# Optimization experiments

Measured on AMD Instinct MI355X. Metric: run time of the kernel, lower is better.

Reference implementation:

```python
import jax, jax.numpy as jnp
import numpy as np
import math

B, L, C, D, H, NLAYERS, DFF = 256, 100, 55, 512, 8, 3, 64


def _pos_embedding(length, d_model):
    pos = np.arange(length, dtype=np.float32)[:, None]
    div = np.exp(np.arange(0, d_model, 2, dtype=np.float32) * (-math.log(10000.0) / d_model))
    pe = np.zeros((length, d_model), dtype=np.float32)
    pe[:, 0::2] = np.sin(pos * div)
    pe[:, 1::2] = np.cos(pos * div)
    return jnp.asarray(pe)


def setup_inputs() -> dict:
    key = jax.random.key(0)
    ks = jax.random.split(key, 12)
    r = lambda k, s, sc: jax.random.normal(k, s, dtype=jnp.float32) * sc
    sD = 1.0 / math.sqrt(D)
    return {
        'x': r(ks[0], (B, L, C), 1.0),
        'tok_w': r(ks[1], (D, C, 3), 1.0 / math.sqrt(3 * C)),  # Conv1d(c_in->d_model, k=3, circular, no bias)
        'pe': _pos_embedding(L, D),
        'Wq': r(ks[2], (NLAYERS, D, D), sD), 'bq': jnp.zeros((NLAYERS, D), jnp.float32),
        'Wk': r(ks[3], (NLAYERS, D, D), sD), 'bk': jnp.zeros((NLAYERS, D), jnp.float32),
        'Wv': r(ks[4], (NLAYERS, D, D), sD), 'bv': jnp.zeros((NLAYERS, D), jnp.float32),
        'Wsig': r(ks[5], (NLAYERS, H, D), sD), 'bsig': jnp.zeros((NLAYERS, H), jnp.float32),
        'Wo': r(ks[6], (NLAYERS, D, D), sD), 'bo': jnp.zeros((NLAYERS, D), jnp.float32),
        'W1': r(ks[7], (NLAYERS, DFF, D), sD), 'b1': jnp.zeros((NLAYERS, DFF), jnp.float32),  # conv1 (1x1)
        'W2': r(ks[8], (NLAYERS, D, DFF), 1.0 / math.sqrt(DFF)), 'b2': jnp.zeros((NLAYERS, D), jnp.float32),  # conv2 (1x1)
        'proj_w': r(ks[9], (C, D), sD), 'proj_b': jnp.zeros((C,), jnp.float32),
    }


def _forward(x, tok_w, pe, Wq, bq, Wk, bk, Wv, bv, Wsig, bsig, Wo, bo, W1, b1, W2, b2, proj_w, proj_b):
    Bx, Lx, _ = x.shape
    nlayers, nH = Wsig.shape[0], Wsig.shape[1]
    d_model = Wq.shape[1]
    dk = d_model // nH
    scale = 1.0 / math.sqrt(dk)
    # token embedding: circular-padded Conv1d(k=3, no bias), then + positional embedding
    xc = jnp.pad(jnp.swapaxes(x, 1, 2), ((0, 0), (0, 0), (1, 1)), mode='wrap')  # [B,C,L+2]
    emb = jax.lax.conv_general_dilated(xc, tok_w, (1,), 'VALID', dimension_numbers=('NCW', 'OIW', 'NCW'))
    h = jnp.swapaxes(emb, 1, 2) + pe[None]  # [B,L,D]
    dist = jnp.abs(jnp.arange(Lx)[:, None] - jnp.arange(Lx)[None, :]).astype(h.dtype)  # |i-j|
    for l in range(nlayers):
        q = h @ Wq[l].T + bq[l]                       # [B,L,D]
        k = (h @ Wk[l].T + bk[l]).reshape(Bx, Lx, nH, dk)
        v = (h @ Wv[l].T + bv[l]).reshape(Bx, Lx, nH, dk)
        # NOTE: source applies sigma projection to the *projected* queries
        sigma = q @ Wsig[l].T + bsig[l]               # [B,L,H]
        qh = q.reshape(Bx, Lx, nH, dk)
        scores = jnp.einsum('blhe,bshe->bhls', qh, k)  # [B,H,L,L]
        series = jax.nn.softmax(scale * scores, axis=-1)
        # Gaussian prior branch (mask_flag=False; computed in source forward,
        # does not feed the module's returned output)
        sg = jnp.swapaxes(sigma, 1, 2)                 # [B,H,L]
        sg = jnp.power(3.0, jax.nn.sigmoid(sg * 5.0) + 1e-5) - 1.0
        sgE = sg[..., None]                            # [B,H,L,1]
        _prior = jnp.exp(-(dist ** 2)[None, None] / (2.0 * sgE ** 2)) / (math.sqrt(2.0 * math.pi) * sgE)
        o = jnp.einsum('bhls,bshd->blhd', series, v).reshape(Bx, Lx, d_model)
        h = h + (o @ Wo[l].T + bo[l])                  # residual 1 (dropout=identity at eval)
        y = jax.nn.gelu(h @ W1[l].T + b1[l], approximate=False)  # conv1 1x1 + gelu
        h = h + (y @ W2[l].T + b2[l])                  # conv2 1x1, residual 2
    return h @ proj_w.T + proj_b                       # [B,L,c_out]


def reference(x, tok_w, pe, Wq, bq, Wk, bk, Wv, bv, Wsig, bsig, Wo, bo, W1, b1, W2, b2, proj_w, proj_b):
    return _forward(x, tok_w, pe, Wq, bq, Wk, bk, Wv, bv, Wsig, bsig, Wo, bo, W1, b1, W2, b2, proj_w, proj_b)
```

## Files before the change

kernel.cpp:

```cpp
#include <hip/hip_runtime.h>
#include <stdint.h>

typedef unsigned short u16;
typedef __attribute__((ext_vector_type(8))) short short8;
typedef __attribute__((ext_vector_type(4))) float f32x4;

#define DEVI __device__ __forceinline__

#define BB   256
#define LL   100
#define CC   55
#define DD   512
#define HH   8
#define DKK  64
#define MM   (BB * LL)
#define KEMB 192
#define NSEG 17

DEVI float bf2f(u16 s) { union { unsigned int u; float f; } x; x.u = ((unsigned int)s) << 16; return x.f; }
DEVI u16 f2bf(float f) {
  union { float f; unsigned int u; } x; x.f = f;
  unsigned int u = x.u;
  return (u16)((u + 0x7FFFu + ((u >> 16) & 1u)) >> 16);
}

DEVI void async_lds16(const u16* gp, u16* lp) {
  __builtin_amdgcn_global_load_lds((const __attribute__((address_space(1))) void*)gp,
                                   (__attribute__((address_space(3))) void*)lp, 16, 0, 0);
}

DEVI void wave_lds_fence() {
  asm volatile("s_waitcnt lgkmcnt(0)" ::: "memory");
  __builtin_amdgcn_wave_barrier();
}

DEVI int swz_row(int r) { return (r & 3) ^ ((r >> 2) & 3); }

__global__ void detect_dtype(const u16* __restrict__ x, int* __restrict__ flag) {
  __shared__ int cnt[256];
  int tid = threadIdx.x;
  u16 u = x[2 * tid];
  int e = (u >> 7) & 0xFF;
  cnt[tid] = (e >= 0x5F && e <= 0x90) ? 1 : 0;
  __syncthreads();
  for (int s = 128; s > 0; s >>= 1) { if (tid < s) cnt[tid] += cnt[tid + s]; __syncthreads(); }
  if (tid == 0) *flag = (cnt[0] >= 160) ? 0 : 1;
}

struct Segs { const void* src[NSEG]; int off[NSEG + 1]; };

__global__ void convert_all(Segs s, const int* __restrict__ flag, u16* __restrict__ dst) {
  int i = blockIdx.x * 256 + threadIdx.x;
  if (i >= s.off[NSEG]) return;
  int sidx = 0;
#pragma unroll
  for (int k = 1; k < NSEG; k++) if (i >= s.off[k]) sidx = k;
  int j = i - s.off[sidx];
  u16 v;
  if (*flag) v = f2bf(((const float*)s.src[sidx])[j]);
  else       v = ((const u16*)s.src[sidx])[j];
  dst[i] = v;
}

__global__ void repack_w(const u16* __restrict__ tokw, u16* __restrict__ Wg) {
  int idx = blockIdx.x * 256 + threadIdx.x;
  if (idx >= 512 * KEMB) return;
  int d = idx / KEMB, j = idx % KEMB, k = j >> 6, c = j & 63;
  Wg[idx] = (c < CC) ? tokw[d * (CC * 3) + c * 3 + k] : (u16)0;
}

__global__ void repack_x(const u16* __restrict__ x, u16* __restrict__ Xg) {
  int idx = blockIdx.x * 256 + threadIdx.x;
  if (idx >= MM * KEMB) return;
  int m = idx / KEMB, j = idx % KEMB, k = j >> 6, c = j & 63;
  int b = m / LL, l = m % LL;
  int l2 = l + k - 1; l2 = (l2 + LL) % LL;
  Xg[idx] = (c < CC) ? x[(size_t)(b * LL + l2) * CC + c] : (u16)0;
}

struct GemmW { const u16* W[3]; const u16* bias[3]; void* out[3]; };

template<int BM, int BN, int NTT, int TAG, bool QKV, bool DIRECT>
__global__ __launch_bounds__(256)
void gemm_bt(const u16* __restrict__ A, int K, GemmW w,
             const u16* __restrict__ pe,
             const u16* __restrict__ resid,
             int dogelu,
             int ldo, int nvalid,
             const int* __restrict__ dtf)
{
  constexpr int BK = 32;
  constexpr int MI = BM / 32;
  constexpr int CW = BN / 2, NT = CW / 16;
  constexpr int SW = CW + 4;
  constexpr int STAGE_U16 = (BM + BN) * BK * 2;
  __shared__ alignas(16) u16 smem[STAGE_U16];
  u16* As = smem;
  u16* Bs = smem + BM * BK * 2;

  const int tid = threadIdx.x;
  const int lane = tid & 63;
  const int wv = __builtin_amdgcn_readfirstlane(tid >> 6);
  const int wm = wv & 1, wn = wv >> 1;
  const int l15 = lane & 15, qd = lane >> 4;
  const int swz = swz_row(l15);

  const int id = blockIdx.x;
  const int mpx = gridDim.x / (NTT * 8);
  const int xcd = id & 7, slot = id >> 3;
  const int m_t = xcd * mpx + slot / NTT;
  const int n_t = slot % NTT;
  const int m0 = m_t * BM;
  int n0 = n_t * BN;
  int sel = 0, n0l = n0;
  if (QKV) { sel = n0 >> 9; n0l = n0 & 511; }
  const u16* W = w.W[sel];
  const u16* bias = w.bias[sel];
  void* outp = w.out[sel];

  const f32x4 zf = {0.f, 0.f, 0.f, 0.f};
  f32x4 acc[MI][NT];
#pragma unroll
  for (int i = 0; i < MI; i++)
#pragma unroll
    for (int j = 0; j < NT; j++) acc[i][j] = zf;

  for (int k0 = 0; k0 < K; k0 += 2 * BK) {
    __syncthreads();
#pragma unroll
    for (int p = 0; p < 2; p++) {
      u16* Asp = As + p * BM * BK;
      u16* Bsp = Bs + p * BN * BK;
      const int kp = k0 + p * BK;
#pragma unroll
      for (int i = 0; i < BM / 64; i++) {
        int base = i * 256 + wv * 64;
        int idx = base + lane;
        int row = idx >> 2;
        int cs = ((idx & 3) ^ swz_row(row)) * 8;
        async_lds16(A + (size_t)(m0 + row) * K + kp + cs, Asp + base * 8);
      }
#pragma unroll
      for (int i = 0; i < BN / 64; i++) {
        int base = i * 256 + wv * 64;
        int idx = base + lane;
        int row = idx >> 2;
        int cs = ((idx & 3) ^ swz_row(row)) * 8;
        int gr = n0l + row; if (gr >= nvalid) gr = nvalid - 1;
        async_lds16(W + (size_t)gr * K + kp + cs, Bsp + base * 8);
      }
    }
    __syncthreads();

#pragma unroll
    for (int p = 0; p < 2; p++) {
      const u16* Asp = As + p * BM * BK;
      const u16* Bsp = Bs + p * BN * BK;
      short8 af[MI], bfr[NT];
#pragma unroll
      for (int mi = 0; mi < MI; mi++)
        af[mi] = *(const short8*)&Asp[(wm * (BM / 2) + mi * 16 + l15) * BK + ((qd ^ swz) * 8)];
#pragma unroll
      for (int ni = 0; ni < NT; ni++)
        bfr[ni] = *(const short8*)&Bsp[(wn * CW + ni * 16 + l15) * BK + ((qd ^ swz) * 8)];
#pragma unroll
      for (int mi = 0; mi < MI; mi++)
#pragma unroll
        for (int ni = 0; ni < NT; ni++)
          acc[mi][ni] = __builtin_amdgcn_mfma_f32_16x16x32_bf16(af[mi], bfr[ni], acc[mi][ni], 0, 0, 0);
    }
  }

  if (DIRECT) {
    const int sf = (dtf != nullptr) ? *dtf : 0;
#pragma unroll
    for (int mi = 0; mi < MI; mi++)
#pragma unroll
      for (int ni = 0; ni < NT; ni++) {
        int gcol = n0l + wn * CW + ni * 16 + l15;
        float bv = (bias && gcol < nvalid) ? bf2f(bias[gcol]) : 0.f;
#pragma unroll
        for (int r = 0; r < 4; r++) {
          int grow = m0 + wm * (BM / 2) + mi * 16 + qd * 4 + r;
          if (gcol < nvalid) {
            float v = acc[mi][ni][r] + bv;
            if (sf) ((float*)outp)[(size_t)grow * ldo + gcol] = v;
            else    ((u16*)outp)[(size_t)grow * ldo + gcol] = f2bf(v);
          }
        }
      }
    return;
  }

  __syncthreads();
  u16* slab = smem + wv * 16 * SW;
#pragma unroll
  for (int mi = 0; mi < MI; mi++) {
    const int lr = wm * (BM / 2) + mi * 16 + qd * 4;
    float v[NT][4];
    if (!QKV && resid) {
#pragma unroll
      for (int ni = 0; ni < NT; ni++) {
        int col = n0l + wn * CW + ni * 16 + l15;
#pragma unroll
        for (int r = 0; r < 4; r++)
          v[ni][r] = bf2f(resid[(size_t)(m0 + lr + r) * DD + col]);
      }
    } else {
#pragma unroll
      for (int ni = 0; ni < NT; ni++)
#pragma unroll
        for (int r = 0; r < 4; r++) v[ni][r] = 0.f;
    }
#pragma unroll
    for (int ni = 0; ni < NT; ni++) {
      const int lc = wn * CW + ni * 16 + l15;
      float bv = bias ? bf2f(bias[n0l + lc]) : 0.f;
#pragma unroll
      for (int r = 0; r < 4; r++) {
        float x = v[ni][r] + acc[mi][ni][r] + bv;
        if (!QKV && pe) x += bf2f(pe[((m0 + lr + r) % LL) * DD + n0l + lc]);
        if (!QKV && dogelu) x = 0.5f * x * (1.f + erff(x * 0.70710678118654752f));
        v[ni][r] = x;
      }
    }
#pragma unroll
    for (int ni = 0; ni < NT; ni++)
#pragma unroll
      for (int r = 0; r < 4; r++)
        slab[(qd * 4 + r) * SW + ni * 16 + l15] = f2bf(v[ni][r]);
    wave_lds_fence();
    if (BN == 128) {
      int r2 = lane >> 2, c2 = (lane & 3) * 16;
      int grow = m0 + wm * (BM / 2) + mi * 16 + r2;
      u16* op = (u16*)outp + (size_t)grow * ldo + n0l + wn * CW + c2;
      *(short8*)&op[0] = *(const short8*)&slab[r2 * SW + c2];
      *(short8*)&op[8] = *(const short8*)&slab[r2 * SW + c2 + 8];
    } else {
      if (lane < 32) {
        int r2 = lane >> 1, c2 = (lane & 1) * 16;
        int grow = m0 + wm * (BM / 2) + mi * 16 + r2;
        u16* op = (u16*)outp + (size_t)grow * ldo + n0l + wn * CW + c2;
        *(short8*)&op[0] = *(const short8*)&slab[r2 * SW + c2];
        *(short8*)&op[8] = *(const short8*)&slab[r2 * SW + c2 + 8];
      }
    }
    wave_lds_fence();
  }
}

__global__ __launch_bounds__(512)
void gemm_qkv(const u16* __restrict__ A, GemmW w)
{
  constexpr int K = DD;
  constexpr int NBK = K >> 5;
  constexpr int SLOT = 12288;
  __shared__ alignas(16) u16 smem[3 * SLOT];

  const int tid = threadIdx.x;
  const int lane = tid & 63;
  const int wv = __builtin_amdgcn_readfirstlane(tid >> 6);
  const int wm = wv & 1, wn = wv >> 1;
  const int l15 = lane & 15, qd = lane >> 4;
  const int swk = ((qd ^ swz_row(l15)) & 3) * 8;

  const int id = blockIdx.x;
  const int mpx = gridDim.x / 48;
  const int xcd = id & 7, sl = id >> 3;
  const int m_t = xcd * mpx + sl / 6;
  const int n_t = sl % 6;
  const int m0 = m_t * 128;
  const int sel = n_t >> 1;
  const int n0l = (n_t & 1) * 256;
  const u16* W = w.W[sel];
  const u16* bias = w.bias[sel];
  u16* outp = (u16*)w.out[sel];

  const int arow = tid >> 2;
  const u16* a_src = A + (size_t)(m0 + arow) * K + ((tid & 3) ^ swz_row(arow)) * 8;
  const int br0 = tid >> 2, br1 = 128 + (tid >> 2);
  const u16* b_src0 = W + (size_t)(n0l + br0) * K + ((tid & 3) ^ swz_row(br0)) * 8;
  const u16* b_src1 = W + (size_t)(n0l + br1) * K + ((tid & 3) ^ swz_row(br1)) * 8;
  const int a_dst  = wv * 512;
  const int b_dst0 = 4096 + wv * 512;
  const int b_dst1 = 8192 + wv * 512;

  auto STAGE = [&](int t) {
    u16* sb = smem + (t % 3) * SLOT;
    const int kp = t << 5;
    async_lds16(a_src + kp,  sb + a_dst);
    async_lds16(b_src0 + kp, sb + b_dst0);
    async_lds16(b_src1 + kp, sb + b_dst1);
  };

  const f32x4 zf = {0.f, 0.f, 0.f, 0.f};
  f32x4 acc[4][4];
#pragma unroll
  for (int i = 0; i < 4; i++)
#pragma unroll
    for (int j = 0; j < 4; j++) acc[i][j] = zf;

  STAGE(0);
  STAGE(1);
  for (int s = 0; s < NBK; ++s) {
    if (s + 1 < NBK) {
      asm volatile("s_waitcnt vmcnt(3)" ::: "memory");
    } else {
      asm volatile("s_waitcnt vmcnt(0)" ::: "memory");
    }
    __builtin_amdgcn_s_barrier();
    asm volatile("" ::: "memory");
    if (s + 2 < NBK) STAGE(s + 2);
    const u16* sb = smem + (s % 3) * SLOT;
    short8 af[4], bf[4];
#pragma unroll
    for (int mi = 0; mi < 4; mi++)
      af[mi] = *(const short8*)&sb[(wm * 64 + mi * 16 + l15) * 32 + swk];
#pragma unroll
    for (int ni = 0; ni < 4; ni++)
      bf[ni] = *(const short8*)&sb[4096 + (wn * 64 + ni * 16 + l15) * 32 + swk];
#pragma unroll
    for (int mi = 0; mi < 4; mi++)
#pragma unroll
      for (int ni = 0; ni < 4; ni++)
        acc[mi][ni] = __builtin_amdgcn_mfma_f32_16x16x32_bf16(af[mi], bf[ni], acc[mi][ni], 0, 0, 0);
    asm volatile("s_waitcnt lgkmcnt(0)" ::: "memory");
  }
  __syncthreads();

  u16* slab = smem + wv * 4608;
#pragma unroll
  for (int mi = 0; mi < 4; mi++)
#pragma unroll
    for (int ni = 0; ni < 4; ni++) {
      float bv = bf2f(bias[n0l + wn * 64 + ni * 16 + l15]);
#pragma unroll
      for (int r = 0; r < 4; r++)
        slab[(mi * 16 + qd * 4 + r) * 72 + ni * 16 + l15] = f2bf(acc[mi][ni][r] + bv);
    }
  wave_lds_fence();
  {
    const int srow = lane >> 3, chk = lane & 7;
#pragma unroll
    for (int j = 0; j < 8; j++) {
      int row = j * 8 + srow;
      int grow = m0 + wm * 64 + row;
      u16* op = outp + (size_t)grow * DD + n0l + wn * 64 + chk * 8;
      *(short8*)op = *(const short8*)&slab[row * 72 + chk * 8];
    }
  }
}

__global__ __launch_bounds__(512)
void gemm_wo(const u16* __restrict__ A, const u16* __restrict__ W,
             const u16* __restrict__ bias, const u16* __restrict__ resid,
             u16* __restrict__ outp)
{
  constexpr int K = DD;
  constexpr int NBK = K >> 5;
  constexpr int SLOT = 8192;
  __shared__ alignas(16) u16 smem[3 * SLOT];

  const int tid = threadIdx.x;
  const int lane = tid & 63;
  const int wv = __builtin_amdgcn_readfirstlane(tid >> 6);
  const int wm = wv & 1, wn = wv >> 1;
  const int l15 = lane & 15, qd = lane >> 4;
  const int swk = ((qd ^ swz_row(l15)) & 3) * 8;

  const int id = blockIdx.x;
  const int mpx = gridDim.x >> 5;
  const int xcd = id & 7, sl = id >> 3;
  const int m_t = xcd * mpx + (sl >> 2);
  const int m0 = m_t * 128;
  const int n0l = (sl & 3) * 128;

  const int prow = tid >> 2;
  const int pcs = ((tid & 3) ^ swz_row(prow)) * 8;
  const u16* a_src = A + (size_t)(m0 + prow) * K + pcs;
  const u16* b_src = W + (size_t)(n0l + prow) * K + pcs;
  const int a_dst = wv * 512;
  const int b_dst = 4096 + wv * 512;

  auto STAGE = [&](int t) {
    u16* sb = smem + (t % 3) * SLOT;
    const int kp = t << 5;
    async_lds16(a_src + kp, sb + a_dst);
    async_lds16(b_src + kp, sb + b_dst);
  };

  const f32x4 zf = {0.f, 0.f, 0.f, 0.f};
  f32x4 acc[4][2];
#pragma unroll
  for (int i = 0; i < 4; i++)
#pragma unroll
    for (int j = 0; j < 2; j++) acc[i][j] = zf;

  STAGE(0);
  STAGE(1);
  for (int s = 0; s < NBK; ++s) {
    if (s + 1 < NBK) {
      asm volatile("s_waitcnt vmcnt(2)" ::: "memory");
    } else {
      asm volatile("s_waitcnt vmcnt(0)" ::: "memory");
    }
    __builtin_amdgcn_s_barrier();
    asm volatile("" ::: "memory");
    if (s + 2 < NBK) STAGE(s + 2);
    const u16* sb = smem + (s % 3) * SLOT;
    short8 af[4], bf[2];
#pragma unroll
    for (int mi = 0; mi < 4; mi++)
      af[mi] = *(const short8*)&sb[(wm * 64 + mi * 16 + l15) * 32 + swk];
#pragma unroll
    for (int ni = 0; ni < 2; ni++)
      bf[ni] = *(const short8*)&sb[4096 + (wn * 32 + ni * 16 + l15) * 32 + swk];
#pragma unroll
    for (int mi = 0; mi < 4; mi++)
#pragma unroll
      for (int ni = 0; ni < 2; ni++)
        acc[mi][ni] = __builtin_amdgcn_mfma_f32_16x16x32_bf16(af[mi], bf[ni], acc[mi][ni], 0, 0, 0);
    asm volatile("s_waitcnt lgkmcnt(0)" ::: "memory");
  }
  __syncthreads();

  u16* slab = smem + wv * 2304;
#pragma unroll
  for (int mi = 0; mi < 4; mi++)
#pragma unroll
    for (int ni = 0; ni < 2; ni++) {
      const int col = n0l + wn * 32 + ni * 16 + l15;
      float bv = bf2f(bias[col]);
#pragma unroll
      for (int r = 0; r < 4; r++) {
        const int grow = m0 + wm * 64 + mi * 16 + qd * 4 + r;
        float x = acc[mi][ni][r] + bv + bf2f(resid[(size_t)grow * DD + col]);
        slab[(mi * 16 + qd * 4 + r) * 36 + ni * 16 + l15] = f2bf(x);
      }
    }
  wave_lds_fence();
  {
    const int srow = lane >> 2, chk = lane & 3;
#pragma unroll
    for (int j = 0; j < 4; j++) {
      int row = j * 16 + srow;
      int grow = m0 + wm * 64 + row;
      u16* op = outp + (size_t)grow * DD + n0l + wn * 32 + chk * 8;
      *(short8*)op = *(const short8*)&slab[row * 36 + chk * 8];
    }
  }
}

__global__ __launch_bounds__(256)
void ffn_fused(const u16* __restrict__ h, const u16* __restrict__ W1,
               const u16* __restrict__ b1, const u16* __restrict__ W2,
               const u16* __restrict__ b2, u16* __restrict__ hout)
{
  constexpr int BM = 64, BK = 32, SW = 36;
  __shared__ alignas(16) u16 smem[4096 + 10496];
  u16* y      = smem;
  u16* shared = smem + 4096;
  u16* As  = shared;
  u16* Bs  = shared + 4096;
  u16* Bs2 = shared;
  u16* slabs = shared + 8192;

  const int tid = threadIdx.x;
  const int lane = tid & 63;
  const int wv = __builtin_amdgcn_readfirstlane(tid >> 6);
  const int wm = wv & 1, wn = wv >> 1;
  const int l15 = lane & 15, qd = lane >> 4;
  const int swz = swz_row(l15);
  const int id = blockIdx.x;
  const int mpx = gridDim.x >> 3;
  const int lid = (id & 7) * mpx + (id >> 3);
  const int m0 = (lid >> 1) * BM;
  const int nh = lid & 1;

  const int srow = tid >> 2;
  const int scs = ((tid & 3) ^ swz_row(srow)) * 8;
  const f32x4 zf = {0.f, 0.f, 0.f, 0.f};

  f32x4 acc[2][2];
#pragma unroll
  for (int i = 0; i < 2; i++)
#pragma unroll
    for (int j = 0; j < 2; j++) acc[i][j] = zf;

  for (int k0 = 0; k0 < DD; k0 += 64) {
    __syncthreads();
#pragma unroll
    for (int p = 0; p < 2; p++) {
      const int kp = k0 + p * BK;
      async_lds16(h  + (size_t)(m0 + srow) * DD + kp + scs, As + p * 2048 + tid * 8);
      async_lds16(W1 + (size_t)srow * DD + kp + scs,        Bs + p * 2048 + tid * 8);
    }
    __syncthreads();
#pragma unroll
    for (int p = 0; p < 2; p++) {
      short8 af[2], bfr[2];
#pragma unroll
      for (int mi = 0; mi < 2; mi++)
        af[mi] = *(const short8*)&As[p * 2048 + (wm * 32 + mi * 16 + l15) * BK + ((qd ^ swz) * 8)];
#pragma unroll
      for (int ni = 0; ni < 2; ni++)
        bfr[ni] = *(const short8*)&Bs[p * 2048 + (wn * 32 + ni * 16 + l15) * BK + ((qd ^ swz) * 8)];
#pragma unroll
      for (int mi = 0; mi < 2; mi++)
#pragma unroll
        for (int ni = 0; ni < 2; ni++)
          acc[mi][ni] = __builtin_amdgcn_mfma_f32_16x16x32_bf16(af[mi], bfr[ni], acc[mi][ni], 0, 0, 0);
    }
  }
#pragma unroll
  for (int mi = 0; mi < 2; mi++)
#pragma unroll
    for (int ni = 0; ni < 2; ni++) {
      float bv = bf2f(b1[wn * 32 + ni * 16 + l15]);
#pragma unroll
      for (int r = 0; r < 4; r++) {
        int row = wm * 32 + mi * 16 + qd * 4 + r;
        int kpos = ni * 16 + l15;
        int slot = ((kpos >> 3) ^ swz_row(row)) & 3;
        float x = acc[mi][ni][r] + bv;
        x = 0.5f * x * (1.f + erff(x * 0.70710678118654752f));
        y[wn * 2048 + row * BK + slot * 8 + (kpos & 7)] = f2bf(x);
      }
    }
  __syncthreads();

  auto stage2 = [&](int buf, int nc) {
#pragma unroll
    for (int p = 0; p < 2; p++)
      async_lds16(W2 + (size_t)(nc * 64 + srow) * 64 + p * BK + scs,
                  Bs2 + buf * 4096 + p * 2048 + tid * 8);
  };
  const int nc0 = nh * 4, nc1 = nc0 + 4;
  stage2(0, nc0);
  int cur = 0;
  u16* slab = slabs + wv * 16 * SW;
  for (int nc = nc0; nc < nc1; nc++) {
    __syncthreads();
    if (nc + 1 < nc1) stage2(cur ^ 1, nc + 1);
    f32x4 a2[2][2];
#pragma unroll
    for (int i = 0; i < 2; i++)
#pragma unroll
      for (int j = 0; j < 2; j++) a2[i][j] = zf;
#pragma unroll
    for (int p = 0; p < 2; p++) {
      short8 af[2], bfr[2];
#pragma unroll
      for (int mi = 0; mi < 2; mi++)
        af[mi] = *(const short8*)&y[p * 2048 + (wm * 32 + mi * 16 + l15) * BK + ((qd ^ swz) * 8)];
#pragma unroll
      for (int ni = 0; ni < 2; ni++)
        bfr[ni] = *(const short8*)&Bs2[cur * 4096 + p * 2048 + (wn * 32 + ni * 16 + l15) * BK + ((qd ^ swz) * 8)];
#pragma unroll
      for (int mi = 0; mi < 2; mi++)
#pragma unroll
        for (int ni = 0; ni < 2; ni++)
          a2[mi][ni] = __builtin_amdgcn_mfma_f32_16x16x32_bf16(af[mi], bfr[ni], a2[mi][ni], 0, 0, 0);
    }
    const int n0l = nc * 64;
#pragma unroll
    for (int mi = 0; mi < 2; mi++) {
      const int lr = wm * 32 + mi * 16 + qd * 4;
      float v[2][4];
#pragma unroll
      for (int ni = 0; ni < 2; ni++) {
        int col = n0l + wn * 32 + ni * 16 + l15;
        float bv = bf2f(b2[col]);
#pragma unroll
        for (int r = 0; r < 4; r++)
          v[ni][r] = bf2f(h[(size_t)(m0 + lr + r) * DD + col]) + a2[mi][ni][r] + bv;
      }
#pragma unroll
      for (int ni = 0; ni < 2; ni++)
#pragma unroll
        for (int r = 0; r < 4; r++)
          slab[(qd * 4 + r) * SW + ni * 16 + l15] = f2bf(v[ni][r]);
      wave_lds_fence();
      if (lane < 32) {
        int r2 = lane >> 1, c2 = (lane & 1) * 16;
        int grow = m0 + wm * 32 + mi * 16 + r2;
        u16* op = hout + (size_t)grow * DD + n0l + wn * 32 + c2;
        *(short8*)&op[0] = *(const short8*)&slab[r2 * SW + c2];
        *(short8*)&op[8] = *(const short8*)&slab[r2 * SW + c2 + 8];
      }
      wave_lds_fence();
    }
    cur ^= 1;
  }
}

__global__ __launch_bounds__(256)
void attn(const u16* __restrict__ qg, const u16* __restrict__ kg,
          const u16* __restrict__ vg, u16* __restrict__ og)
{
  constexpr int LP = 128;
  __shared__ alignas(16) u16 Ks[LP * DKK];
  __shared__ alignas(16) u16 Vt[DKK * LP];

  const int bh = blockIdx.x;
  const int b = bh >> 3, h = bh & 7;
  const size_t base = (size_t)b * LL * DD + (size_t)h * DKK;
  const int tid = threadIdx.x, lane = tid & 63, wv = tid >> 6;
  const int l15 = lane & 15, qd = lane >> 4;
  const short8 z8 = {0, 0, 0, 0, 0, 0, 0, 0};

  for (int i = tid; i < LP * 8; i += 256) {
    int row = i >> 3, e8 = (i & 7) * 8;
    short8 val = z8;
    if (row < LL) val = *(const short8*)(kg + base + (size_t)row * DD + e8);
    *(short8*)&Ks[row * DKK + e8] = val;
  }
  for (int i = tid; i < LP * 8; i += 256) {
    int j = i & 127, d0 = (i >> 7) * 8;
    short8 val = z8;
    if (j < LL) val = *(const short8*)(vg + base + (size_t)j * DD + d0);
#pragma unroll
    for (int u = 0; u < 8; u++) Vt[(d0 + u) * LP + j] = (u16)val[u];
  }
  __syncthreads();

  const f32x4 zf = {0.f, 0.f, 0.f, 0.f};
  f32x4 sc[2][8];
#pragma unroll
  for (int it = 0; it < 2; it++)
#pragma unroll
    for (int jt = 0; jt < 8; jt++) sc[it][jt] = zf;

  short8 af[2][2];
#pragma unroll
  for (int it = 0; it < 2; it++) {
    int row = (2 * wv + it) * 16 + l15;
#pragma unroll
    for (int ks = 0; ks < 2; ks++) {
      short8 val = z8;
      if (row < LL) val = *(const short8*)(qg + base + (size_t)row * DD + ks * 32 + qd * 8);
      af[it][ks] = val;
    }
  }
#pragma unroll
  for (int jt = 0; jt < 8; jt++) {
    short8 b0 = *(const short8*)&Ks[(jt * 16 + l15) * DKK + qd * 8];
    short8 b1 = *(const short8*)&Ks[(jt * 16 + l15) * DKK + 32 + qd * 8];
#pragma unroll
    for (int it = 0; it < 2; it++) {
      sc[it][jt] = __builtin_amdgcn_mfma_f32_16x16x32_bf16(af[it][0], b0, sc[it][jt], 0, 0, 0);
      sc[it][jt] = __builtin_amdgcn_mfma_f32_16x16x32_bf16(af[it][1], b1, sc[it][jt], 0, 0, 0);
    }
  }

  constexpr float scale = 0.125f;
#pragma unroll
  for (int it = 0; it < 2; it++) {
#pragma unroll
    for (int r = 0; r < 4; r++) {
      float vals[8];
      float mx = -1e30f;
#pragma unroll
      for (int jt = 0; jt < 8; jt++) {
        int col = jt * 16 + l15;
        float vv = sc[it][jt][r] * scale;
        if (col >= LL) vv = -1e30f;
        vals[jt] = vv;
        mx = fmaxf(mx, vv);
      }
#pragma unroll
      for (int off = 1; off < 16; off <<= 1) mx = fmaxf(mx, __shfl_xor(mx, off, 64));
      float s = 0.f;
#pragma unroll
      for (int jt = 0; jt < 8; jt++) { float p = __expf(vals[jt] - mx); vals[jt] = p; s += p; }
#pragma unroll
      for (int off = 1; off < 16; off <<= 1) s += __shfl_xor(s, off, 64);
      float inv = 1.f / s;
#pragma unroll
      for (int jt = 0; jt < 8; jt++) sc[it][jt][r] = vals[jt] * inv;
    }
  }
  __syncthreads();

  u16* Pc = Ks;
  f32x4 oc[2][4];
#pragma unroll
  for (int it = 0; it < 2; it++)
#pragma unroll
    for (int dt = 0; dt < 4; dt++) oc[it][dt] = zf;

#pragma unroll
  for (int it = 0; it < 2; it++) {
    int rb = (2 * wv + it) * 16 + qd * 4;
#pragma unroll
    for (int r = 0; r < 4; r++)
#pragma unroll
      for (int jt = 0; jt < 4; jt++)
        Pc[(rb + r) * DKK + jt * 16 + l15] = f2bf(sc[it][jt][r]);
  }
  __syncthreads();
#pragma unroll
  for (int ks = 0; ks < 2; ks++) {
    short8 ap[2];
#pragma unroll
    for (int it = 0; it < 2; it++)
      ap[it] = *(const short8*)&Pc[((2 * wv + it) * 16 + l15) * DKK + ks * 32 + qd * 8];
#pragma unroll
    for (int dt = 0; dt < 4; dt++) {
      short8 bv = *(const short8*)&Vt[(dt * 16 + l15) * LP + ks * 32 + qd * 8];
#pragma unroll
      for (int it = 0; it < 2; it++)
        oc[it][dt] = __builtin_amdgcn_mfma_f32_16x16x32_bf16(ap[it], bv, oc[it][dt], 0, 0, 0);
    }
  }
  __syncthreads();

#pragma unroll
  for (int it = 0; it < 2; it++) {
    int rb = (2 * wv + it) * 16 + qd * 4;
#pragma unroll
    for (int r = 0; r < 4; r++)
#pragma unroll
      for (int jt = 4; jt < 8; jt++)
        Pc[(rb + r) * DKK + (jt - 4) * 16 + l15] = f2bf(sc[it][jt][r]);
  }
  __syncthreads();
#pragma unroll
  for (int ks = 2; ks < 4; ks++) {
    short8 ap[2];
#pragma unroll
    for (int it = 0; it < 2; it++)
      ap[it] = *(const short8*)&Pc[((2 * wv + it) * 16 + l15) * DKK + (ks - 2) * 32 + qd * 8];
#pragma unroll
    for (int dt = 0; dt < 4; dt++) {
      short8 bv = *(const short8*)&Vt[(dt * 16 + l15) * LP + ks * 32 + qd * 8];
#pragma unroll
      for (int it = 0; it < 2; it++)
        oc[it][dt] = __builtin_amdgcn_mfma_f32_16x16x32_bf16(ap[it], bv, oc[it][dt], 0, 0, 0);
    }
  }

  __syncthreads();
  u16* Os = Ks;
#pragma unroll
  for (int it = 0; it < 2; it++) {
    int rb = (2 * wv + it) * 16 + qd * 4;
#pragma unroll
    for (int dt = 0; dt < 4; dt++)
#pragma unroll
      for (int r = 0; r < 4; r++)
        Os[(rb + r) * DKK + dt * 16 + l15] = f2bf(oc[it][dt][r]);
  }
  __syncthreads();
  {
    int row = tid >> 1, c0 = (tid & 1) * 32;
    if (row < LL) {
      u16* op = og + base + (size_t)row * DD + c0;
#pragma unroll
      for (int c = 0; c < 32; c += 8)
        *(short8*)&op[c] = *(const short8*)&Os[row * DKK + c0 + c];
    }
  }
}

extern "C" void kernel_launch(void* const* d_in, const int* in_sizes, int n_in,
                              void* d_out, int out_size, void* d_ws, size_t ws_size,
                              hipStream_t stream)
{
  (void)in_sizes; (void)n_in; (void)out_size; (void)ws_size;

  char* ws = (char*)d_ws;
  size_t off = 0;
  auto alloc = [&](size_t bytes) { char* p = ws + off; off += (bytes + 255) & ~(size_t)255; return p; };
  int* dflag = (int*)alloc(256);
  static const int seg_sizes[NSEG] = {
    MM * CC, DD * CC * 3, LL * DD,
    3 * DD * DD, 3 * DD, 3 * DD * DD, 3 * DD, 3 * DD * DD, 3 * DD,
    3 * DD * DD, 3 * DD, 3 * 64 * DD, 3 * 64, 3 * DD * 64, 3 * DD,
    CC * DD, CC
  };
  static const int seg_input[NSEG] = {0, 1, 2, 3, 4, 5, 6, 7, 8, 11, 12, 13, 14, 15, 16, 17, 18};
  int total = 0, segoff[NSEG + 1];
  for (int i = 0; i < NSEG; i++) { segoff[i] = total; total += seg_sizes[i]; }
  segoff[NSEG] = total;
  u16* canon = (u16*)alloc((size_t)total * 2);

  u16* hbf = (u16*)alloc((size_t)MM * DD * 2);
  u16* h2  = (u16*)alloc((size_t)MM * DD * 2);
  u16* qb  = (u16*)alloc((size_t)MM * DD * 2);
  u16* kb  = (u16*)alloc((size_t)MM * DD * 2);
  u16* vb  = (u16*)alloc((size_t)MM * DD * 2);
  u16* ob  = (u16*)alloc((size_t)MM * DD * 2);
  u16* Wg  = (u16*)alloc((size_t)512 * KEMB * 2);
  u16* Xg  = qb;

  const u16* xc  = canon + segoff[0];
  const u16* twc = canon + segoff[1];
  const u16* pec = canon + segoff[2];
  const u16* Wqc = canon + segoff[3];  const u16* bqc = canon + segoff[4];
  const u16* Wkc = canon + segoff[5];  const u16* bkc = canon + segoff[6];
  const u16* Wvc = canon + segoff[7];  const u16* bvc = canon + segoff[8];
  const u16* Woc = canon + segoff[9];  const u16* boc = canon + segoff[10];
  const u16* W1c = canon + segoff[11]; const u16* b1c = canon + segoff[12];
  const u16* W2c = canon + segoff[13]; const u16* b2c = canon + segoff[14];
  const u16* pwc = canon + segoff[15]; const u16* pbc = canon + segoff[16];

  Segs sg;
  for (int i = 0; i < NSEG; i++) { sg.src[i] = d_in[seg_input[i]]; sg.off[i] = segoff[i]; }
  sg.off[NSEG] = total;

  dim3 blk(256);
  detect_dtype<<<dim3(1), blk, 0, stream>>>((const u16*)d_in[0], dflag);
  convert_all<<<dim3((total + 255) / 256), blk, 0, stream>>>(sg, dflag, canon);
  repack_w<<<dim3((512 * KEMB + 255) / 256), blk, 0, stream>>>(twc, Wg);
  repack_x<<<dim3((MM * KEMB + 255) / 256), blk, 0, stream>>>(xc, Xg);

  auto W1of = [&](const u16* p) { GemmW g{}; g.W[0] = g.W[1] = g.W[2] = p; return g; };

  { GemmW g = W1of(Wg); g.out[0] = hbf;
    gemm_bt<128, 64, 8, 0, false, false><<<dim3(1600), blk, 0, stream>>>(Xg, KEMB, g, pec, nullptr, 0, DD, DD, nullptr); }

  u16* hc = hbf;
  for (int l = 0; l < 3; l++) {
    const u16* Wq_l = Wqc + (size_t)l * DD * DD; const u16* bq_l = bqc + l * DD;
    const u16* Wk_l = Wkc + (size_t)l * DD * DD; const u16* bk_l = bkc + l * DD;
    const u16* Wv_l = Wvc + (size_t)l * DD * DD; const u16* bv_l = bvc + l * DD;
    const u16* Wo_l = Woc + (size_t)l * DD * DD; const u16* bo_l = boc + l * DD;
    const u16* W1_l = W1c + (size_t)l * 64 * DD; const u16* b1_l = b1c + l * 64;
    const u16* W2_l = W2c + (size_t)l * DD * 64; const u16* b2_l = b2c + l * DD;

    { GemmW g{}; g.W[0] = Wq_l; g.W[1] = Wk_l; g.W[2] = Wv_l;
      g.bias[0] = bq_l; g.bias[1] = bk_l; g.bias[2] = bv_l;
      g.out[0] = qb; g.out[1] = kb; g.out[2] = vb;
      gemm_qkv<<<dim3(1200), dim3(512), 0, stream>>>(hc, g); }

    attn<<<dim3(BB * HH), blk, 0, stream>>>(qb, kb, vb, ob);

    gemm_wo<<<dim3(800), dim3(512), 0, stream>>>(ob, Wo_l, bo_l, hc, hc);

    u16* hn = (hc == hbf) ? h2 : hbf;
    ffn_fused<<<dim3(800), blk, 0, stream>>>(hc, W1_l, b1_l, W2_l, b2_l, hn);
    hc = hn;
  }
  { GemmW g = W1of(pwc); g.bias[0] = pbc; g.out[0] = d_out;
    gemm_bt<64, 64, 1, 5, false, true><<<dim3(400), blk, 0, stream>>>(hc, DD, g, nullptr, nullptr, 0, CC, CC, dflag); }
}
```

Measured before the change: 570.6 us.

## Pipeline FFN first GEMM with a three-slot async LDS ring buffer

Replaces the synchronous load-then-compute loop in the FFN's first GEMM (two barriers per 64-wide K step) with a 3-deep ring of 32-wide K slices. Loads are issued two stages ahead and consumption is gated by vmcnt waits plus a single barrier per step. The goal is to overlap global-to-LDS transfers with MFMA work and halve the barrier count, at the cost of more LDS and hand-managed waitcnt ordering.

New measurement: 567.0 us. About the same (-0.6%).

```diff
diff --git a/kernel.cpp b/kernel.cpp
--- a/kernel.cpp
+++ b/kernel.cpp
@@ -456,14 +456,14 @@
                const u16* __restrict__ b1, const u16* __restrict__ W2,
                const u16* __restrict__ b2, u16* __restrict__ hout)
 {
-  constexpr int BM = 64, BK = 32, SW = 36;
-  __shared__ alignas(16) u16 smem[4096 + 10496];
-  u16* y      = smem;
-  u16* shared = smem + 4096;
-  u16* As  = shared;
-  u16* Bs  = shared + 4096;
-  u16* Bs2 = shared;
-  u16* slabs = shared + 8192;
+  constexpr int BK = 32, SW = 36;
+  constexpr int NBK = DD >> 5;
+  constexpr int SLOT = 4096;
+  __shared__ alignas(16) u16 smem[16896];
+  u16* y     = smem;
+  u16* ring  = smem + 4096;
+  u16* Bs2   = smem + 4096;
+  u16* slabs = smem + 12288;
 
   const int tid = threadIdx.x;
   const int lane = tid & 63;
@@ -471,46 +471,57 @@
   const int wm = wv & 1, wn = wv >> 1;
   const int l15 = lane & 15, qd = lane >> 4;
   const int swz = swz_row(l15);
+  const int swk = ((qd ^ swz) & 3) * 8;
   const int id = blockIdx.x;
   const int mpx = gridDim.x >> 3;
   const int lid = (id & 7) * mpx + (id >> 3);
-  const int m0 = (lid >> 1) * BM;
+  const int m0 = (lid >> 1) * 64;
   const int nh = lid & 1;
 
-  const int srow = tid >> 2;
-  const int scs = ((tid & 3) ^ swz_row(srow)) * 8;
+  const int prow = tid >> 2;
+  const int pcs = ((tid & 3) ^ swz_row(prow)) * 8;
+  const u16* a_src = h  + (size_t)(m0 + prow) * DD + pcs;
+  const u16* b_src = W1 + (size_t)prow * DD + pcs;
   const f32x4 zf = {0.f, 0.f, 0.f, 0.f};
 
+  auto STAGE1 = [&](int t) {
+    u16* sb = ring + (t % 3) * SLOT;
+    const int kp = t << 5;
+    async_lds16(a_src + kp, sb + wv * 512);
+    async_lds16(b_src + kp, sb + 2048 + wv * 512);
+  };
+
   f32x4 acc[2][2];
 #pragma unroll
   for (int i = 0; i < 2; i++)
 #pragma unroll
     for (int j = 0; j < 2; j++) acc[i][j] = zf;
 
-  for (int k0 = 0; k0 < DD; k0 += 64) {
-    __syncthreads();
-#pragma unroll
-    for (int p = 0; p < 2; p++) {
-      const int kp = k0 + p * BK;
-      async_lds16(h  + (size_t)(m0 + srow) * DD + kp + scs, As + p * 2048 + tid * 8);
-      async_lds16(W1 + (size_t)srow * DD + kp + scs,        Bs + p * 2048 + tid * 8);
-    }
-    __syncthreads();
-#pragma unroll
-    for (int p = 0; p < 2; p++) {
-      short8 af[2], bfr[2];
-#pragma unroll
-      for (int mi = 0; mi < 2; mi++)
-        af[mi] = *(const short8*)&As[p * 2048 + (wm * 32 + mi * 16 + l15) * BK + ((qd ^ swz) * 8)];
+  STAGE1(0);
+  STAGE1(1);
+  for (int s = 0; s < NBK; ++s) {
+    if (s + 1 < NBK) {
+      asm volatile("s_waitcnt vmcnt(2)" ::: "memory");
+    } else {
+      asm volatile("s_waitcnt vmcnt(0)" ::: "memory");
+    }
+    __builtin_amdgcn_s_barrier();
+    asm volatile("" ::: "memory");
+    if (s + 2 < NBK) STAGE1(s + 2);
+    const u16* sb = ring + (s % 3) * SLOT;
+    short8 af[2], bfr[2];
+#pragma unroll
+    for (int mi = 0; mi < 2; mi++)
+      af[mi] = *(const short8*)&sb[(wm * 32 + mi * 16 + l15) * BK + swk];
+#pragma unroll
+    for (int ni = 0; ni < 2; ni++)
+      bfr[ni] = *(const short8*)&sb[2048 + (wn * 32 + ni * 16 + l15) * BK + swk];
+#pragma unroll
+    for (int mi = 0; mi < 2; mi++)
 #pragma unroll
       for (int ni = 0; ni < 2; ni++)
-        bfr[ni] = *(const short8*)&Bs[p * 2048 + (wn * 32 + ni * 16 + l15) * BK + ((qd ^ swz) * 8)];
-#pragma unroll
-      for (int mi = 0; mi < 2; mi++)
-#pragma unroll
-        for (int ni = 0; ni < 2; ni++)
-          acc[mi][ni] = __builtin_amdgcn_mfma_f32_16x16x32_bf16(af[mi], bfr[ni], acc[mi][ni], 0, 0, 0);
-    }
+        acc[mi][ni] = __builtin_amdgcn_mfma_f32_16x16x32_bf16(af[mi], bfr[ni], acc[mi][ni], 0, 0, 0);
+    asm volatile("s_waitcnt lgkmcnt(0)" ::: "memory");
   }
 #pragma unroll
   for (int mi = 0; mi < 2; mi++)
@@ -532,7 +543,7 @@
   auto stage2 = [&](int buf, int nc) {
 #pragma unroll
     for (int p = 0; p < 2; p++)
-      async_lds16(W2 + (size_t)(nc * 64 + srow) * 64 + p * BK + scs,
+      async_lds16(W2 + (size_t)(nc * 64 + prow) * 64 + p * BK + pcs,
                   Bs2 + buf * 4096 + p * 2048 + tid * 8);
   };
   const int nc0 = nh * 4, nc1 = nc0 + 4;
```
